# Optimization experiments

Hardware: AMD Instinct MI355X
Metric: run time of the kernel (lower is better)

## Reference

```python
import jax, jax.numpy as jnp
import numpy as np

B, L, D = 64, 512, 768
KSIZE, PAD = 3, 1
BN_EPS = 1e-5
COS_EPS = 1e-8

def _gauss_kernel(kernel_size, sigma, k):
    X = np.linspace(-k, k, kernel_size)
    x, y = np.meshgrid(X, X)
    g = 1.0 / (2 * np.pi * sigma ** 2) * np.exp(-(x ** 2 + y ** 2) / (2 * sigma ** 2))
    return g.astype(np.float32)

def setup_inputs() -> dict:
    key = jax.random.key(0)
    k1, k2, k3, k4 = jax.random.split(key, 4)
    news = jax.random.normal(k1, (B, L, D), dtype=jnp.float32)
    post = jax.random.normal(k2, (B, L, D), dtype=jnp.float32)
    gauss_kernel = jnp.asarray(_gauss_kernel(KSIZE, 2, 1))[None, None]  # (1,1,3,3), frozen
    bn_gamma = jnp.ones((1,), jnp.float32)
    bn_beta = jnp.zeros((1,), jnp.float32)
    bound = 1.0 / np.sqrt(L)
    lin_w = jax.random.uniform(k3, (L, L), jnp.float32, -bound, bound)
    lin_b = jax.random.uniform(k4, (L,), jnp.float32, -bound, bound)
    return {"news": news, "post": post, "gauss_kernel": gauss_kernel,
            "bn_gamma": bn_gamma, "bn_beta": bn_beta, "lin_w": lin_w, "lin_b": lin_b}

def reference(news, post, gauss_kernel, bn_gamma, bn_beta, lin_w, lin_b):
    # cosine similarity along feature dim (torch eps semantics)
    nn_ = jnp.maximum(jnp.linalg.norm(news, axis=-1), COS_EPS)
    np_ = jnp.maximum(jnp.linalg.norm(post, axis=-1), COS_EPS)
    cos = jnp.sum(news * post, axis=-1) / (nn_ * np_)           # (B, L)
    # the original loop writes the same cos row into every i -> broadcast
    trans = jnp.broadcast_to(cos[:, None, :], (cos.shape[0], cos.shape[1], cos.shape[1]))
    x = trans[:, None]                                           # (B,1,L,L)
    wk = jax.lax.conv_general_dilated(
        x, gauss_kernel, window_strides=(1, 1),
        padding=[(PAD, PAD), (PAD, PAD)],
        dimension_numbers=("NCHW", "OIHW", "NCHW"))             # (B,1,L,L)
    # BatchNorm2d(1) in training mode: batch stats over (N,H,W)
    mu = jnp.mean(wk)
    var = jnp.mean((wk - mu) ** 2)
    wk = (wk - mu) * jax.lax.rsqrt(var + BN_EPS) * bn_gamma[0] + bn_beta[0]
    wk = wk[:, 0]                                                # (B,L,L)
    wk = jnp.einsum("blm,nm->bln", wk, lin_w) + lin_b            # Linear over last dim
    wk = jax.nn.softmax(wk, axis=-2).sum(axis=-1)[..., None]     # (B,L,1)
    word_feat = (wk * news).mean(axis=1)                         # (B,D)
    post_feat = (wk * post).mean(axis=1)[:, None]                # (B,1,D)
    return (word_feat, post_feat)
```

## Files before the change

### kernel.cpp

```cpp
#include <hip/hip_runtime.h>
#include <math.h>

#define NB 64
#define NL 512
#define ND 768

static constexpr float kCosEps = 1e-8f;
static constexpr double kBnEps = 1e-5;

static constexpr size_t OFF_ACC = 0;
static constexpr size_t OFF_CSN = 256;
static constexpr size_t SZ_PART = (size_t)8 * NB * ND * 4;
static constexpr size_t OFF_CSP = OFF_CSN + SZ_PART;
static constexpr size_t OFF_COS = OFF_CSP + SZ_PART;
static constexpr size_t SZ_BL   = (size_t)NB * NL * 4;
static constexpr size_t OFF_HI  = OFF_COS + SZ_BL;
static constexpr size_t OFF_HT  = OFF_HI + SZ_BL;
static constexpr size_t OFF_HB  = OFF_HT + SZ_BL;
static constexpr size_t OFF_ABC = OFF_HB + SZ_BL;

__global__ __launch_bounds__(256) void k1_cos_colsum(
    const float* __restrict__ news, const float* __restrict__ post,
    float* __restrict__ cosv, float* __restrict__ csn_part,
    float* __restrict__ csp_part)
{
    __shared__ float lds_n[4][ND];
    __shared__ float lds_p[4][ND];
    const int b    = blockIdx.x >> 3;
    const int tile = blockIdx.x & 7;
    const int tid  = threadIdx.x;
    const int wave = tid >> 6;
    const int lane = tid & 63;

    float an[12], ap[12];
#pragma unroll
    for (int k = 0; k < 12; ++k) { an[k] = 0.f; ap[k] = 0.f; }

    for (int r = 0; r < 16; ++r) {
        const int l = tile * 64 + r * 4 + wave;
        const float4* nrow = (const float4*)(news + ((size_t)b * NL + l) * ND);
        const float4* prow = (const float4*)(post + ((size_t)b * NL + l) * ND);
        float nn = 0.f, pp = 0.f, npd = 0.f;
#pragma unroll
        for (int k = 0; k < 3; ++k) {
            const float4 nv = nrow[lane + 64 * k];
            const float4 pv = prow[lane + 64 * k];
            nn  += nv.x * nv.x + nv.y * nv.y + nv.z * nv.z + nv.w * nv.w;
            pp  += pv.x * pv.x + pv.y * pv.y + pv.z * pv.z + pv.w * pv.w;
            npd += nv.x * pv.x + nv.y * pv.y + nv.z * pv.z + nv.w * pv.w;
            an[4 * k + 0] += nv.x; an[4 * k + 1] += nv.y;
            an[4 * k + 2] += nv.z; an[4 * k + 3] += nv.w;
            ap[4 * k + 0] += pv.x; ap[4 * k + 1] += pv.y;
            ap[4 * k + 2] += pv.z; ap[4 * k + 3] += pv.w;
        }
#pragma unroll
        for (int m = 32; m >= 1; m >>= 1) {
            nn  += __shfl_xor(nn, m);
            pp  += __shfl_xor(pp, m);
            npd += __shfl_xor(npd, m);
        }
        if (lane == 0) {
            const float dn = fmaxf(sqrtf(nn), kCosEps) * fmaxf(sqrtf(pp), kCosEps);
            cosv[b * NL + l] = npd / dn;
        }
    }
#pragma unroll
    for (int k = 0; k < 3; ++k) {
        const int d0 = 4 * (lane + 64 * k);
        lds_n[wave][d0 + 0] = an[4 * k + 0]; lds_n[wave][d0 + 1] = an[4 * k + 1];
        lds_n[wave][d0 + 2] = an[4 * k + 2]; lds_n[wave][d0 + 3] = an[4 * k + 3];
        lds_p[wave][d0 + 0] = ap[4 * k + 0]; lds_p[wave][d0 + 1] = ap[4 * k + 1];
        lds_p[wave][d0 + 2] = ap[4 * k + 2]; lds_p[wave][d0 + 3] = ap[4 * k + 3];
    }
    __syncthreads();
    float* outn = csn_part + ((size_t)tile * NB + b) * ND;
    float* outp = csp_part + ((size_t)tile * NB + b) * ND;
    for (int i = tid; i < ND; i += 256) {
        outn[i] = lds_n[0][i] + lds_n[1][i] + lds_n[2][i] + lds_n[3][i];
        outp[i] = lds_p[0][i] + lds_p[1][i] + lds_p[2][i] + lds_p[3][i];
    }
}

__global__ __launch_bounds__(256) void k2_conv_stats(
    const float* __restrict__ cosv, const float* __restrict__ g,
    float* __restrict__ hi, float* __restrict__ ht, float* __restrict__ hb,
    double* __restrict__ acc)
{
    __shared__ float row[NL + 2];
    __shared__ double sred[8];
    const int b   = blockIdx.x;
    const int tid = threadIdx.x;
    if (tid == 0) { row[0] = 0.f; row[NL + 1] = 0.f; }
    for (int j = tid; j < NL; j += 256) row[j + 1] = cosv[b * NL + j];
    __syncthreads();

    const float ci0 = g[0] + g[3] + g[6], ci1 = g[1] + g[4] + g[7], ci2 = g[2] + g[5] + g[8];
    const float ct0 = g[3] + g[6],        ct1 = g[4] + g[7],        ct2 = g[5] + g[8];
    const float cb0 = g[0] + g[3],        cb1 = g[1] + g[4],        cb2 = g[2] + g[5];

    double s = 0.0, s2 = 0.0;
    for (int j = tid; j < NL; j += 256) {
        const float a = row[j], c = row[j + 1], d = row[j + 2];
        const float vi = ci0 * a + ci1 * c + ci2 * d;
        const float vt = ct0 * a + ct1 * c + ct2 * d;
        const float vb = cb0 * a + cb1 * c + cb2 * d;
        hi[b * NL + j] = vi; ht[b * NL + j] = vt; hb[b * NL + j] = vb;
        s  += (double)vi * (NL - 2) + (double)vt + (double)vb;
        s2 += (double)vi * vi * (NL - 2) + (double)vt * vt + (double)vb * vb;
    }
    const int lane = tid & 63, wave = tid >> 6;
#pragma unroll
    for (int m = 32; m >= 1; m >>= 1) { s += __shfl_xor(s, m); s2 += __shfl_xor(s2, m); }
    if (lane == 0) { sred[wave] = s; sred[4 + wave] = s2; }
    __syncthreads();
    if (tid == 0) {
        atomicAdd(&acc[0], sred[0] + sred[1] + sred[2] + sred[3]);
        atomicAdd(&acc[1], sred[4] + sred[5] + sred[6] + sred[7]);
    }
}

__global__ __launch_bounds__(256) void k3_linear_softmax(
    const float* __restrict__ hi, const float* __restrict__ ht,
    const float* __restrict__ hb, const float* __restrict__ W,
    const float* __restrict__ bias, const float* __restrict__ gamma,
    const float* __restrict__ beta, const double* __restrict__ acc,
    float* __restrict__ abc)
{
    __shared__ float shi[NL], sht[NL], shb[NL];
    __shared__ float sred[12];
    const int b   = blockIdx.x;
    const int tid = threadIdx.x;

    const double N   = (double)NB * NL * NL;
    const double mu  = acc[0] / N;
    const double var = acc[1] / N - mu * mu;
    const float  sc  = gamma[0] * (float)(1.0 / sqrt(var + kBnEps));
    const float  sh  = beta[0] - (float)mu * sc;

    for (int j = tid; j < NL; j += 256) {
        shi[j] = hi[b * NL + j] * sc + sh;
        sht[j] = ht[b * NL + j] * sc + sh;
        shb[j] = hb[b * NL + j] * sc + sh;
    }
    __syncthreads();

    const float4* s4i = (const float4*)shi;
    const float4* s4t = (const float4*)sht;
    const float4* s4b = (const float4*)shb;

    float sa = 0.f, st = 0.f, sb = 0.f;
    for (int n = tid; n < NL; n += 256) {
        const float4* wr = (const float4*)(W + (size_t)n * NL);
        float zi = 0.f, zt = 0.f, zb = 0.f;
        for (int m = 0; m < NL / 4; ++m) {
            const float4 w  = wr[m];
            const float4 vi = s4i[m], vt = s4t[m], vb = s4b[m];
            zi += w.x * vi.x + w.y * vi.y + w.z * vi.z + w.w * vi.w;
            zt += w.x * vt.x + w.y * vt.y + w.z * vt.z + w.w * vt.w;
            zb += w.x * vb.x + w.y * vb.y + w.z * vb.z + w.w * vb.w;
        }
        const float bv = bias[n];
        zi += bv; zt += bv; zb += bv;
        const float M  = fmaxf(zi, fmaxf(zt, zb));
        const float ei = expf(zi - M), et = expf(zt - M), eb = expf(zb - M);
        const float r  = 1.f / ((float)(NL - 2) * ei + et + eb);
        sa += ei * r; st += et * r; sb += eb * r;
    }
    const int lane = tid & 63, wave = tid >> 6;
#pragma unroll
    for (int m = 32; m >= 1; m >>= 1) {
        sa += __shfl_xor(sa, m); st += __shfl_xor(st, m); sb += __shfl_xor(sb, m);
    }
    if (lane == 0) { sred[wave * 3] = sa; sred[wave * 3 + 1] = st; sred[wave * 3 + 2] = sb; }
    __syncthreads();
    if (tid == 0) {
        abc[b * 3 + 0] = sred[0] + sred[3] + sred[6] + sred[9];
        abc[b * 3 + 1] = sred[1] + sred[4] + sred[7] + sred[10];
        abc[b * 3 + 2] = sred[2] + sred[5] + sred[8] + sred[11];
    }
}

__global__ __launch_bounds__(256) void k4_out(
    const float* __restrict__ news, const float* __restrict__ post,
    const float* __restrict__ csn_part, const float* __restrict__ csp_part,
    const float* __restrict__ abc, float* __restrict__ out)
{
    const int idx = blockIdx.x * 256 + threadIdx.x;
    if (idx >= NB * ND) return;
    const int b = idx / ND, d = idx - b * ND;
    const float a  = abc[b * 3 + 0];
    const float ct = abc[b * 3 + 1];
    const float cb = abc[b * 3 + 2];
    float cn = 0.f, cp = 0.f;
#pragma unroll
    for (int t = 0; t < 8; ++t) {
        cn += csn_part[((size_t)t * NB + b) * ND + d];
        cp += csp_part[((size_t)t * NB + b) * ND + d];
    }
    const size_t base = (size_t)b * NL * ND;
    const float n0 = news[base + d], nL = news[base + (size_t)(NL - 1) * ND + d];
    const float p0 = post[base + d], pL = post[base + (size_t)(NL - 1) * ND + d];
    const float invL = 1.f / NL;
    out[idx]           = (a * cn + (ct - a) * n0 + (cb - a) * nL) * invL;
    out[NB * ND + idx] = (a * cp + (ct - a) * p0 + (cb - a) * pL) * invL;
}

extern "C" void kernel_launch(void* const* d_in, const int* in_sizes, int n_in,
                              void* d_out, int out_size, void* d_ws, size_t ws_size,
                              hipStream_t stream) {
    const float* news     = (const float*)d_in[0];
    const float* post     = (const float*)d_in[1];
    const float* g        = (const float*)d_in[2];
    const float* bn_gamma = (const float*)d_in[3];
    const float* bn_beta  = (const float*)d_in[4];
    const float* lin_w    = (const float*)d_in[5];
    const float* lin_b    = (const float*)d_in[6];
    float* out = (float*)d_out;
    char*  ws  = (char*)d_ws;

    double* acc = (double*)(ws + OFF_ACC);
    float* csn  = (float*)(ws + OFF_CSN);
    float* csp  = (float*)(ws + OFF_CSP);
    float* cosv = (float*)(ws + OFF_COS);
    float* hi   = (float*)(ws + OFF_HI);
    float* ht   = (float*)(ws + OFF_HT);
    float* hb   = (float*)(ws + OFF_HB);
    float* abc  = (float*)(ws + OFF_ABC);

    hipMemsetAsync(acc, 0, 2 * sizeof(double), stream);

    k1_cos_colsum<<<NB * 8, 256, 0, stream>>>(news, post, cosv, csn, csp);
    k2_conv_stats<<<NB, 256, 0, stream>>>(cosv, g, hi, ht, hb, acc);
    k3_linear_softmax<<<NB, 256, 0, stream>>>(hi, ht, hb, lin_w, lin_b,
                                              bn_gamma, bn_beta, acc, abc);
    k4_out<<<192, 256, 0, stream>>>(news, post, csn, csp, abc, out);
}
```

Measured before the change: 92.45 us.

## Double-buffer k1 row loads via global_load_lds and atomically accumulate column sums

Rewrites the cosine/column-sum kernel to stage rows into LDS with asynchronous global-to-LDS loads, double-buffered so the next chunk's load overlaps compute on the current one. It doubles the grid to 16 tiles per batch and defers the wave reductions to batch them at the end. Per-tile partial column sums become float atomicAdds into a single zeroed buffer, which removes the 8-way partial reduction in the output kernel. The cost is a larger memset, atomic contention and non-deterministic summation order.

```diff
diff --git a/kernel.cpp b/kernel.cpp
--- a/kernel.cpp
+++ b/kernel.cpp
@@ -10,74 +10,120 @@
 
 static constexpr size_t OFF_ACC = 0;
 static constexpr size_t OFF_CSN = 256;
-static constexpr size_t SZ_PART = (size_t)8 * NB * ND * 4;
-static constexpr size_t OFF_CSP = OFF_CSN + SZ_PART;
-static constexpr size_t OFF_COS = OFF_CSP + SZ_PART;
+static constexpr size_t SZ_CS   = (size_t)NB * ND * 4;
+static constexpr size_t OFF_CSP = OFF_CSN + SZ_CS;
+static constexpr size_t MEMSET_BYTES = OFF_CSP + SZ_CS;
+static constexpr size_t OFF_COS = 393728;
 static constexpr size_t SZ_BL   = (size_t)NB * NL * 4;
 static constexpr size_t OFF_HI  = OFF_COS + SZ_BL;
 static constexpr size_t OFF_HT  = OFF_HI + SZ_BL;
 static constexpr size_t OFF_HB  = OFF_HT + SZ_BL;
 static constexpr size_t OFF_ABC = OFF_HB + SZ_BL;
 
+__device__ __forceinline__ float dot4(float4 a, float4 b) {
+    return a.x * b.x + a.y * b.y + a.z * b.z + a.w * b.w;
+}
+
+#define GLD16(ldst, gsrc)                                                        \
+    __builtin_amdgcn_global_load_lds(                                            \
+        (const __attribute__((address_space(1))) void*)(gsrc),                   \
+        (__attribute__((address_space(3))) void*)(ldst), 16, 0, 0)
+
 __global__ __launch_bounds__(256) void k1_cos_colsum(
     const float* __restrict__ news, const float* __restrict__ post,
-    float* __restrict__ cosv, float* __restrict__ csn_part,
-    float* __restrict__ csp_part)
-{
-    __shared__ float lds_n[4][ND];
-    __shared__ float lds_p[4][ND];
-    const int b    = blockIdx.x >> 3;
-    const int tile = blockIdx.x & 7;
+    float* __restrict__ cosv, float* __restrict__ csn,
+    float* __restrict__ csp)
+{
+    __shared__ float stage[2][8 * ND];
+    const int b    = blockIdx.x >> 4;
+    const int t16  = blockIdx.x & 15;
+    const int l0   = t16 * 32;
     const int tid  = threadIdx.x;
     const int wave = tid >> 6;
     const int lane = tid & 63;
 
+    const float* nbase = news + ((size_t)b * NL + l0 + wave) * ND + lane * 4;
+    const float* pbase = post + ((size_t)b * NL + l0 + wave) * ND + lane * 4;
+
+    float nn[8], pp[8], npd[8];
     float an[12], ap[12];
 #pragma unroll
     for (int k = 0; k < 12; ++k) { an[k] = 0.f; ap[k] = 0.f; }
 
-    for (int r = 0; r < 16; ++r) {
-        const int l = tile * 64 + r * 4 + wave;
-        const float4* nrow = (const float4*)(news + ((size_t)b * NL + l) * ND);
-        const float4* prow = (const float4*)(post + ((size_t)b * NL + l) * ND);
-        float nn = 0.f, pp = 0.f, npd = 0.f;
-#pragma unroll
-        for (int k = 0; k < 3; ++k) {
-            const float4 nv = nrow[lane + 64 * k];
-            const float4 pv = prow[lane + 64 * k];
-            nn  += nv.x * nv.x + nv.y * nv.y + nv.z * nv.z + nv.w * nv.w;
-            pp  += pv.x * pv.x + pv.y * pv.y + pv.z * pv.z + pv.w * pv.w;
-            npd += nv.x * pv.x + nv.y * pv.y + nv.z * pv.z + nv.w * pv.w;
-            an[4 * k + 0] += nv.x; an[4 * k + 1] += nv.y;
-            an[4 * k + 2] += nv.z; an[4 * k + 3] += nv.w;
-            ap[4 * k + 0] += pv.x; ap[4 * k + 1] += pv.y;
-            ap[4 * k + 2] += pv.z; ap[4 * k + 3] += pv.w;
-        }
-#pragma unroll
-        for (int m = 32; m >= 1; m >>= 1) {
-            nn  += __shfl_xor(nn, m);
-            pp  += __shfl_xor(pp, m);
-            npd += __shfl_xor(npd, m);
-        }
-        if (lane == 0) {
-            const float dn = fmaxf(sqrtf(nn), kCosEps) * fmaxf(sqrtf(pp), kCosEps);
-            cosv[b * NL + l] = npd / dn;
-        }
-    }
 #pragma unroll
     for (int k = 0; k < 3; ++k) {
-        const int d0 = 4 * (lane + 64 * k);
-        lds_n[wave][d0 + 0] = an[4 * k + 0]; lds_n[wave][d0 + 1] = an[4 * k + 1];
-        lds_n[wave][d0 + 2] = an[4 * k + 2]; lds_n[wave][d0 + 3] = an[4 * k + 3];
-        lds_p[wave][d0 + 0] = ap[4 * k + 0]; lds_p[wave][d0 + 1] = ap[4 * k + 1];
-        lds_p[wave][d0 + 2] = ap[4 * k + 2]; lds_p[wave][d0 + 3] = ap[4 * k + 3];
-    }
-    __syncthreads();
-    float* outn = csn_part + ((size_t)tile * NB + b) * ND;
-    float* outp = csp_part + ((size_t)tile * NB + b) * ND;
+        GLD16(&stage[0][wave * ND + k * 256],       nbase + k * 256);
+        GLD16(&stage[0][(4 + wave) * ND + k * 256], pbase + k * 256);
+    }
+    __syncthreads();
+
+    for (int c = 0; c < 8; ++c) {
+        const int cur = c & 1;
+        if (c < 7) {
+            const int nxt = cur ^ 1;
+            const size_t goff = (size_t)(c + 1) * 4 * ND;
+#pragma unroll
+            for (int k = 0; k < 3; ++k) {
+                GLD16(&stage[nxt][wave * ND + k * 256],       nbase + goff + k * 256);
+                GLD16(&stage[nxt][(4 + wave) * ND + k * 256], pbase + goff + k * 256);
+            }
+        }
+        const float4* ln = (const float4*)&stage[cur][wave * ND];
+        const float4* lp = (const float4*)&stage[cur][(4 + wave) * ND];
+        const float4 A0 = ln[lane], A1 = ln[lane + 64], A2 = ln[lane + 128];
+        const float4 B0 = lp[lane], B1 = lp[lane + 64], B2 = lp[lane + 128];
+
+        nn[c]  = dot4(A0, A0) + dot4(A1, A1) + dot4(A2, A2);
+        pp[c]  = dot4(B0, B0) + dot4(B1, B1) + dot4(B2, B2);
+        npd[c] = dot4(A0, B0) + dot4(A1, B1) + dot4(A2, B2);
+
+        an[0] += A0.x; an[1] += A0.y; an[2]  += A0.z; an[3]  += A0.w;
+        an[4] += A1.x; an[5] += A1.y; an[6]  += A1.z; an[7]  += A1.w;
+        an[8] += A2.x; an[9] += A2.y; an[10] += A2.z; an[11] += A2.w;
+        ap[0] += B0.x; ap[1] += B0.y; ap[2]  += B0.z; ap[3]  += B0.w;
+        ap[4] += B1.x; ap[5] += B1.y; ap[6]  += B1.z; ap[7]  += B1.w;
+        ap[8] += B2.x; ap[9] += B2.y; ap[10] += B2.z; ap[11] += B2.w;
+
+        __syncthreads();
+    }
+
+#pragma unroll
+    for (int m = 1; m <= 32; m <<= 1) {
+#pragma unroll
+        for (int c = 0; c < 8; ++c) {
+            nn[c]  += __shfl_xor(nn[c], m);
+            pp[c]  += __shfl_xor(pp[c], m);
+            npd[c] += __shfl_xor(npd[c], m);
+        }
+    }
+    if (lane == 0) {
+#pragma unroll
+        for (int c = 0; c < 8; ++c) {
+            const float dn = fmaxf(sqrtf(nn[c]), kCosEps) * fmaxf(sqrtf(pp[c]), kCosEps);
+            cosv[b * NL + l0 + c * 4 + wave] = npd[c] / dn;
+        }
+    }
+
+    {
+        float4* wn = (float4*)&stage[0][wave * ND];
+        float4* wp = (float4*)&stage[0][(4 + wave) * ND];
+        wn[lane]       = make_float4(an[0], an[1], an[2], an[3]);
+        wn[lane + 64]  = make_float4(an[4], an[5], an[6], an[7]);
+        wn[lane + 128] = make_float4(an[8], an[9], an[10], an[11]);
+        wp[lane]       = make_float4(ap[0], ap[1], ap[2], ap[3]);
+        wp[lane + 64]  = make_float4(ap[4], ap[5], ap[6], ap[7]);
+        wp[lane + 128] = make_float4(ap[8], ap[9], ap[10], ap[11]);
+    }
+    __syncthreads();
     for (int i = tid; i < ND; i += 256) {
-        outn[i] = lds_n[0][i] + lds_n[1][i] + lds_n[2][i] + lds_n[3][i];
-        outp[i] = lds_p[0][i] + lds_p[1][i] + lds_p[2][i] + lds_p[3][i];
+        float sn = 0.f, sp = 0.f;
+#pragma unroll
+        for (int w = 0; w < 4; ++w) {
+            sn += stage[0][w * ND + i];
+            sp += stage[0][(4 + w) * ND + i];
+        }
+        atomicAdd(&csn[b * ND + i], sn);
+        atomicAdd(&csp[b * ND + i], sp);
     }
 }
 
@@ -182,7 +228,7 @@
 
 __global__ __launch_bounds__(256) void k4_out(
     const float* __restrict__ news, const float* __restrict__ post,
-    const float* __restrict__ csn_part, const float* __restrict__ csp_part,
+    const float* __restrict__ csn, const float* __restrict__ csp,
     const float* __restrict__ abc, float* __restrict__ out)
 {
     const int idx = blockIdx.x * 256 + threadIdx.x;
@@ -191,12 +237,8 @@
     const float a  = abc[b * 3 + 0];
     const float ct = abc[b * 3 + 1];
     const float cb = abc[b * 3 + 2];
-    float cn = 0.f, cp = 0.f;
-#pragma unroll
-    for (int t = 0; t < 8; ++t) {
-        cn += csn_part[((size_t)t * NB + b) * ND + d];
-        cp += csp_part[((size_t)t * NB + b) * ND + d];
-    }
+    const float cn = csn[idx];
+    const float cp = csp[idx];
     const size_t base = (size_t)b * NL * ND;
     const float n0 = news[base + d], nL = news[base + (size_t)(NL - 1) * ND + d];
     const float p0 = post[base + d], pL = post[base + (size_t)(NL - 1) * ND + d];
@@ -227,9 +269,9 @@
     float* hb   = (float*)(ws + OFF_HB);
     float* abc  = (float*)(ws + OFF_ABC);
 
-    hipMemsetAsync(acc, 0, 2 * sizeof(double), stream);
-
-    k1_cos_colsum<<<NB * 8, 256, 0, stream>>>(news, post, cosv, csn, csp);
+    hipMemsetAsync(ws, 0, MEMSET_BYTES, stream);
+
+    k1_cos_colsum<<<NB * 16, 256, 0, stream>>>(news, post, cosv, csn, csp);
     k2_conv_stats<<<NB, 256, 0, stream>>>(cosv, g, hi, ht, hb, acc);
     k3_linear_softmax<<<NB, 256, 0, stream>>>(hi, ht, hb, lin_w, lin_b,
                                               bn_gamma, bn_beta, acc, abc);
```

After: 91.75 us. About the same (-0.8%).
